# Kernel optimization log

Hardware: AMD Instinct MI355X
Metric: run time of the kernel (lower is better)

Reference implementation:

```python
import jax, jax.numpy as jnp
import numpy as np

B = 8192          # graphs
A = 1024          # atoms per graph
F = 32            # max fragments per graph
N = B * A
VIRTUAL_IDX = 4   # HPARAMS.get_node_idx('ligand_virtual')


def setup_inputs() -> dict:
    key = jax.random.key(0)
    k1, k2, k3, k4 = jax.random.split(key, 4)
    pos = jax.random.normal(k1, (N, 3), dtype=jnp.float32) * 10.0
    # -1 marks non-ligand atoms (no fragment), as in frag_idx_map semantics
    frag_idx_map = jax.random.randint(k2, (N,), -1, F, dtype=jnp.int32)
    batch_idx = (jnp.arange(N, dtype=jnp.int32) // A).astype(jnp.int32)
    node_entity = jax.random.randint(k3, (N,), 0, 6, dtype=jnp.int32)
    mask = jax.random.bernoulli(k4, 0.95, (N,))
    return {"pos": pos, "frag_idx_map": frag_idx_map, "batch_idx": batch_idx,
            "node_entity": node_entity, "mask": mask,
            "num_graphs": B, "max_frags_per_graph": F}


def reference(pos, frag_idx_map, batch_idx, node_entity, mask,
              num_graphs, max_frags_per_graph):
    """Fused equivalent of get_flat_fragment_index + get_fragment_com.

    Returns (coms [B*F, 3], counts [B*F], flat_frag_idx [N]).
    Rows of coms beyond a graph's actual fragment count are zero-padded.
    """
    Bn = num_graphs
    Fm = max_frags_per_graph
    is_ligand = frag_idx_map >= 0

    # num_frags_per_graph[i] = max(frag_idx in graph i) + 1 (0 if none)
    fmax = jax.ops.segment_max(jnp.where(is_ligand, frag_idx_map, -1),
                               batch_idx, num_segments=Bn)
    nfrag = jnp.maximum(fmax, -1) + 1  # [B]
    offset = jnp.concatenate([jnp.zeros((1,), nfrag.dtype),
                              jnp.cumsum(nfrag)[:-1]])  # [B]

    # flat fragment index in [0, sum(F_i)), -1 for non-ligand atoms
    flat_frag_idx = jnp.where(is_ligand,
                              frag_idx_map + offset[batch_idx],
                              -1)

    # COM excludes virtual nodes and masked dummies
    valid = is_ligand & mask & (node_entity != VIRTUAL_IDX)
    n_seg = Bn * Fm
    seg = jnp.where(valid, flat_frag_idx, n_seg)  # dump invalid into trash segment
    w = valid.astype(pos.dtype)
    sums = jax.ops.segment_sum(pos * w[:, None], seg, num_segments=n_seg + 1)[:-1]
    cnt = jax.ops.segment_sum(w, seg, num_segments=n_seg + 1)[:-1]
    coms = sums / jnp.maximum(cnt, 1.0)[:, None]
    return coms, cnt, flat_frag_idx
```

## Files before the change

kernel.cpp:

```cpp
#include <hip/hip_runtime.h>

#define GA 1024
#define GF 32
#define VIRT 4
#define KG 16

typedef _Float16 half8 __attribute__((ext_vector_type(8)));
typedef float f32x4 __attribute__((ext_vector_type(4)));
typedef unsigned int uint4v __attribute__((ext_vector_type(4)));

#define XSTRIDE 2080
#define KOFF    (4 * XSTRIDE)
#define FOFF    (KOFF + GA)
#define LDSSZ   (FOFF + 4 * GF * 4 * 4)

__device__ __forceinline__ unsigned int h2(float a, float b) {
    const unsigned short lo = __builtin_bit_cast(unsigned short, (_Float16)a);
    const unsigned short hi = __builtin_bit_cast(unsigned short, (_Float16)b);
    return (unsigned int)lo | ((unsigned int)hi << 16);
}

__global__ __launch_bounds__(256) void k_graph_acc(
    const float* __restrict__ pos,
    const int*   __restrict__ frag,
    const int*   __restrict__ entity,
    const int*   __restrict__ mask,
    float*       __restrict__ sums_cnt,
    int*         __restrict__ nfrag,
    unsigned*    __restrict__ frag8u)
{
    const int g    = blockIdx.x;
    const int t    = threadIdx.x;
    const int lane = t & 63;
    const int w    = t >> 6;

    __shared__ alignas(16) unsigned char lds[LDSSZ];
    __shared__ int s_wmax[4];

    const int i0 = g * GA + t * 4;
    const int4  f4 = *(const int4*)(frag   + i0);
    const int4  e4 = *(const int4*)(entity + i0);
    const int4  m4 = *(const int4*)(mask   + i0);
    const float4* p4 = (const float4*)(pos + (size_t)3 * i0);
    const float4 pa = p4[0], pb = p4[1], pc = p4[2];

    if (frag8u) {
        const unsigned s8p = (f4.x & 0xFFu)         | ((f4.y & 0xFFu) << 8)
                           | ((f4.z & 0xFFu) << 16) | ((unsigned)(f4.w & 0xFFu) << 24);
        frag8u[(size_t)g * (GA / 4) + t] = s8p;
    }

    #define KEY(F,M,E) ((unsigned)(((F) >= 0 && (M) != 0 && (E) != VIRT) ? (unsigned)(F) : 0xFFu))
    const unsigned kp = KEY(f4.x,m4.x,e4.x)        | (KEY(f4.y,m4.y,e4.y) << 8)
                      | (KEY(f4.z,m4.z,e4.z) << 16) | (KEY(f4.w,m4.w,e4.w) << 24);
    *(unsigned*)(lds + KOFF + t * 4) = kp;
    #undef KEY

    *(uint2*)(lds + 0 * XSTRIDE + t * 8) = make_uint2(h2(pa.x, pa.w), h2(pb.z, pc.y));
    *(uint2*)(lds + 1 * XSTRIDE + t * 8) = make_uint2(h2(pa.y, pb.x), h2(pb.w, pc.z));
    *(uint2*)(lds + 2 * XSTRIDE + t * 8) = make_uint2(h2(pa.z, pb.y), h2(pc.x, pc.w));
    *(uint2*)(lds + 3 * XSTRIDE + t * 8) = make_uint2(0x3C003C00u, 0x3C003C00u);

    int lm = max(max(f4.x, f4.y), max(f4.z, f4.w));
    #pragma unroll
    for (int off = 32; off > 0; off >>= 1)
        lm = max(lm, __shfl_down(lm, off, 64));
    if (lane == 0) s_wmax[w] = lm;

    f32x4 acc0 = {0.f, 0.f, 0.f, 0.f};
    f32x4 acc1 = {0.f, 0.f, 0.f, 0.f};
    const int row = lane & 15;
    const int grp = lane >> 4;
    const unsigned xoff = (unsigned)((row & 3) * XSTRIDE + (w * 256 + grp * 8) * 2);
    const unsigned koff = (unsigned)(KOFF + w * 256 + grp * 8);

    #pragma unroll
    for (int s = 0; s < 8; ++s) {
        const uint2  kk = *(const uint2*)(lds + koff + s * 32);
        const uint4v bv = *(const uint4v*)(lds + xoff + s * 64);
        uint4v a0, a1;
        #pragma unroll
        for (int p = 0; p < 4; ++p) {
            const unsigned word = (p & 2) ? kk.y : kk.x;
            const unsigned k0 = (word >> ((p & 1) * 16)) & 0xFFu;
            const unsigned k1 = (word >> ((p & 1) * 16 + 8)) & 0xFFu;
            a0[p] = (k0 == (unsigned)row        ? 0x3C00u : 0u)
                  | (k1 == (unsigned)row        ? 0x3C000000u : 0u);
            a1[p] = (k0 == (unsigned)(row + 16) ? 0x3C00u : 0u)
                  | (k1 == (unsigned)(row + 16) ? 0x3C000000u : 0u);
        }
        acc0 = __builtin_amdgcn_mfma_f32_16x16x32_f16(
                   __builtin_bit_cast(half8, a0), __builtin_bit_cast(half8, bv), acc0, 0, 0, 0);
        acc1 = __builtin_amdgcn_mfma_f32_16x16x32_f16(
                   __builtin_bit_cast(half8, a1), __builtin_bit_cast(half8, bv), acc1, 0, 0, 0);
    }

    float* fold = (float*)(lds + FOFF);
    if (row < 4) {
        #pragma unroll
        for (int r = 0; r < 4; ++r) {
            fold[(w * GF + grp * 4 + r) * 4 + row]      = acc0[r];
            fold[(w * GF + 16 + grp * 4 + r) * 4 + row] = acc1[r];
        }
    }
    __syncthreads();
    if (t < GF * 4) {
        const float v = fold[t] + fold[128 + t] + fold[256 + t] + fold[384 + t];
        sums_cnt[(size_t)g * (GF * 4) + t] = v;
    }
    if (t == 0)
        nfrag[g] = max(max(s_wmax[0], s_wmax[1]), max(s_wmax[2], s_wmax[3])) + 1;
}

__global__ __launch_bounds__(256) void k_fin(
    const int*      __restrict__ nfrag,
    const float4*   __restrict__ sums_cnt,
    const unsigned* __restrict__ frag8u,
    const int4*     __restrict__ frag4,
    float*          __restrict__ coms,
    float*          __restrict__ cnt_out,
    float4*         __restrict__ out4,
    int B)
{
    const int b = blockIdx.x;
    const int t = threadIdx.x;
    const int C = B / 256;
    __shared__ int s[8192 + 256];
    __shared__ int ps[256];

    for (int k = 0; k < C; ++k) {
        const int idx = k * 256 + t;
        s[idx + (idx >> 5)] = nfrag[idx];
    }
    __syncthreads();
    int sum = 0;
    for (int k = 0; k < C; ++k) {
        const int idx = t * C + k;
        const int p = idx + (idx >> 5);
        const int v = s[p];
        s[p] = sum;
        sum += v;
    }
    ps[t] = sum;
    __syncthreads();
    for (int d = 1; d < 256; d <<= 1) {
        const int v = (t >= d) ? ps[t - d] : 0;
        __syncthreads();
        ps[t] += v;
        __syncthreads();
    }
    #define OFF(g) (s[(g) + ((g) >> 5)] + (((g) >> 5) ? ps[((g) >> 5) - 1] : 0))
    const int total = ps[255];

    const int g0 = b * KG;

    #pragma unroll
    for (int k = 0; k < (KG * GF) / 256; ++k) {
        const int e  = k * 256 + t;
        const int j  = e >> 5, fr = e & 31;
        const int g  = g0 + j;
        if (fr < nfrag[g]) {
            const float4 v = sums_cnt[(size_t)g * GF + fr];
            const int rr = OFF(g) + fr;
            const float inv = 1.0f / fmaxf(v.w, 1.0f);
            coms[3 * rr + 0] = v.x * inv;
            coms[3 * rr + 1] = v.y * inv;
            coms[3 * rr + 2] = v.z * inv;
            cnt_out[rr] = v.w;
        }
    }

    #pragma unroll
    for (int k = 0; k < 2; ++k) {
        const int r = b * 512 + k * 256 + t;
        if (r >= total) {
            coms[3 * r + 0] = 0.0f; coms[3 * r + 1] = 0.0f; coms[3 * r + 2] = 0.0f;
            cnt_out[r] = 0.0f;
        }
    }

    for (int j = 0; j < KG; ++j) {
        const int g = g0 + j;
        const float fo = (float)OFF(g);
        float4 o;
        if (frag8u) {
            const unsigned kk = frag8u[(size_t)g * (GA / 4) + t];
            const int a0 = ((int)(kk << 24)) >> 24;
            const int a1 = ((int)(kk << 16)) >> 24;
            const int a2 = ((int)(kk <<  8)) >> 24;
            const int a3 = ((int)kk) >> 24;
            o.x = (a0 >= 0) ? (float)a0 + fo : -1.0f;
            o.y = (a1 >= 0) ? (float)a1 + fo : -1.0f;
            o.z = (a2 >= 0) ? (float)a2 + fo : -1.0f;
            o.w = (a3 >= 0) ? (float)a3 + fo : -1.0f;
        } else {
            const int4 f = frag4[(size_t)g * (GA / 4) + t];
            o.x = (f.x >= 0) ? (float)f.x + fo : -1.0f;
            o.y = (f.y >= 0) ? (float)f.y + fo : -1.0f;
            o.z = (f.z >= 0) ? (float)f.z + fo : -1.0f;
            o.w = (f.w >= 0) ? (float)f.w + fo : -1.0f;
        }
        out4[(size_t)g * (GA / 4) + t] = o;
    }
    #undef OFF
}

extern "C" void kernel_launch(void* const* d_in, const int* in_sizes, int n_in,
                              void* d_out, int out_size, void* d_ws, size_t ws_size,
                              hipStream_t stream)
{
    const float* pos    = (const float*)d_in[0];
    const int*   frag   = (const int*)d_in[1];
    const int*   entity = (const int*)d_in[3];
    const int*   mask   = (const int*)d_in[4];

    const int N = in_sizes[1];
    const int B = N / GA;

    float*    sums_cnt = (float*)d_ws;
    int*      nfrag    = (int*)(sums_cnt + (size_t)B * GF * 4);
    unsigned* frag8u   = (unsigned*)(nfrag + B);
    const size_t needed = (size_t)B * GF * 4 * 4 + (size_t)B * 4 + (size_t)N;
    if (ws_size < needed) frag8u = nullptr;

    float* coms     = (float*)d_out;
    float* cnt_out  = coms + (size_t)B * GF * 3;
    float* flat_out = cnt_out + (size_t)B * GF;

    k_graph_acc<<<B, 256, 0, stream>>>(pos, frag, entity, mask, sums_cnt, nfrag, frag8u);

    k_fin<<<B / KG, 256, 0, stream>>>(
        nfrag, (const float4*)sums_cnt, (const unsigned*)frag8u, (const int4*)frag,
        coms, cnt_out, (float4*)flat_out, B);
}
```

Before: 259.8 us.

## Process four graphs per block with register prefetch and atomic per-wave accumulation

Each block of the accumulation kernel now handles four consecutive graphs. While one graph is being processed, the loads for the next graph are issued into registers, so global loads overlap with the MFMA work. The LDS fold and its __syncthreads are gone: each wave atomically adds its partial sums into a workspace that a new memset clears first, and each wave writes its own max fragment index, which the finalize kernel reduces. This adds global atomics, an extra memset launch and a wider nfrag array in exchange for less block synchronization and better latency hiding.

```diff
diff --git a/kernel.cpp b/kernel.cpp
--- a/kernel.cpp
+++ b/kernel.cpp
@@ -3,6 +3,7 @@
 #define GA 1024
 #define GF 32
 #define VIRT 4
+#define NG 4
 #define KG 16
 
 typedef _Float16 half8 __attribute__((ext_vector_type(8)));
@@ -11,8 +12,7 @@
 
 #define XSTRIDE 2080
 #define KOFF    (4 * XSTRIDE)
-#define FOFF    (KOFF + GA)
-#define LDSSZ   (FOFF + 4 * GF * 4 * 4)
+#define LDSSZ   (KOFF + GA)
 
 __device__ __forceinline__ unsigned int h2(float a, float b) {
     const unsigned short lo = __builtin_bit_cast(unsigned short, (_Float16)a);
@@ -20,100 +20,111 @@
     return (unsigned int)lo | ((unsigned int)hi << 16);
 }
 
-__global__ __launch_bounds__(256) void k_graph_acc(
+__global__ __launch_bounds__(256, 8) void k_graph_acc(
     const float* __restrict__ pos,
     const int*   __restrict__ frag,
     const int*   __restrict__ entity,
     const int*   __restrict__ mask,
     float*       __restrict__ sums_cnt,
-    int*         __restrict__ nfrag,
+    int*         __restrict__ nfrag4,
     unsigned*    __restrict__ frag8u)
 {
-    const int g    = blockIdx.x;
     const int t    = threadIdx.x;
     const int lane = t & 63;
     const int w    = t >> 6;
+    const int g0   = blockIdx.x * NG;
 
     __shared__ alignas(16) unsigned char lds[LDSSZ];
-    __shared__ int s_wmax[4];
-
-    const int i0 = g * GA + t * 4;
-    const int4  f4 = *(const int4*)(frag   + i0);
-    const int4  e4 = *(const int4*)(entity + i0);
-    const int4  m4 = *(const int4*)(mask   + i0);
-    const float4* p4 = (const float4*)(pos + (size_t)3 * i0);
-    const float4 pa = p4[0], pb = p4[1], pc = p4[2];
-
-    if (frag8u) {
-        const unsigned s8p = (f4.x & 0xFFu)         | ((f4.y & 0xFFu) << 8)
-                           | ((f4.z & 0xFFu) << 16) | ((unsigned)(f4.w & 0xFFu) << 24);
-        frag8u[(size_t)g * (GA / 4) + t] = s8p;
-    }
-
-    #define KEY(F,M,E) ((unsigned)(((F) >= 0 && (M) != 0 && (E) != VIRT) ? (unsigned)(F) : 0xFFu))
-    const unsigned kp = KEY(f4.x,m4.x,e4.x)        | (KEY(f4.y,m4.y,e4.y) << 8)
-                      | (KEY(f4.z,m4.z,e4.z) << 16) | (KEY(f4.w,m4.w,e4.w) << 24);
-    *(unsigned*)(lds + KOFF + t * 4) = kp;
-    #undef KEY
-
-    *(uint2*)(lds + 0 * XSTRIDE + t * 8) = make_uint2(h2(pa.x, pa.w), h2(pb.z, pc.y));
-    *(uint2*)(lds + 1 * XSTRIDE + t * 8) = make_uint2(h2(pa.y, pb.x), h2(pb.w, pc.z));
-    *(uint2*)(lds + 2 * XSTRIDE + t * 8) = make_uint2(h2(pa.z, pb.y), h2(pc.x, pc.w));
-    *(uint2*)(lds + 3 * XSTRIDE + t * 8) = make_uint2(0x3C003C00u, 0x3C003C00u);
-
-    int lm = max(max(f4.x, f4.y), max(f4.z, f4.w));
-    #pragma unroll
-    for (int off = 32; off > 0; off >>= 1)
-        lm = max(lm, __shfl_down(lm, off, 64));
-    if (lane == 0) s_wmax[w] = lm;
-
-    f32x4 acc0 = {0.f, 0.f, 0.f, 0.f};
-    f32x4 acc1 = {0.f, 0.f, 0.f, 0.f};
+
     const int row = lane & 15;
     const int grp = lane >> 4;
-    const unsigned xoff = (unsigned)((row & 3) * XSTRIDE + (w * 256 + grp * 8) * 2);
-    const unsigned koff = (unsigned)(KOFF + w * 256 + grp * 8);
+    const unsigned xo_l = (unsigned)((row & 3) * XSTRIDE + (w * 256 + grp * 8) * 2);
+    const unsigned ko_l = (unsigned)(KOFF + w * 256 + grp * 8);
+
+    int4 f4, e4, m4; float4 pa, pb, pc;
+    {
+        const size_t i0 = (size_t)g0 * GA + t * 4;
+        f4 = *(const int4*)(frag   + i0);
+        e4 = *(const int4*)(entity + i0);
+        m4 = *(const int4*)(mask   + i0);
+        const float4* p4 = (const float4*)(pos + 3 * i0);
+        pa = p4[0]; pb = p4[1]; pc = p4[2];
+    }
 
     #pragma unroll
-    for (int s = 0; s < 8; ++s) {
-        const uint2  kk = *(const uint2*)(lds + koff + s * 32);
-        const uint4v bv = *(const uint4v*)(lds + xoff + s * 64);
-        uint4v a0, a1;
+    for (int it = 0; it < NG; ++it) {
+        const int g = g0 + it;
+        const int4  cf = f4, ce = e4, cm = m4;
+        const float4 qa = pa, qb = pb, qc = pc;
+
+        if (it + 1 < NG) {
+            const size_t i0 = (size_t)(g + 1) * GA + t * 4;
+            f4 = *(const int4*)(frag   + i0);
+            e4 = *(const int4*)(entity + i0);
+            m4 = *(const int4*)(mask   + i0);
+            const float4* p4 = (const float4*)(pos + 3 * i0);
+            pa = p4[0]; pb = p4[1]; pc = p4[2];
+        }
+
+        if (frag8u) {
+            const unsigned s8p = (cf.x & 0xFFu)         | ((cf.y & 0xFFu) << 8)
+                               | ((cf.z & 0xFFu) << 16) | ((unsigned)(cf.w & 0xFFu) << 24);
+            frag8u[(size_t)g * (GA / 4) + t] = s8p;
+        }
+
+        #define KEYV(F,M,E) ((unsigned)(((F) >= 0 && (M) != 0 && (E) != VIRT) ? (unsigned)(F) : 0xFFu))
+        const unsigned kp = KEYV(cf.x,cm.x,ce.x)        | (KEYV(cf.y,cm.y,ce.y) << 8)
+                          | (KEYV(cf.z,cm.z,ce.z) << 16) | (KEYV(cf.w,cm.w,ce.w) << 24);
+        *(unsigned*)(lds + KOFF + t * 4) = kp;
+        #undef KEYV
+
+        *(uint2*)(lds + 0 * XSTRIDE + t * 8) = make_uint2(h2(qa.x, qa.w), h2(qb.z, qc.y));
+        *(uint2*)(lds + 1 * XSTRIDE + t * 8) = make_uint2(h2(qa.y, qb.x), h2(qb.w, qc.z));
+        *(uint2*)(lds + 2 * XSTRIDE + t * 8) = make_uint2(h2(qa.z, qb.y), h2(qc.x, qc.w));
+        *(uint2*)(lds + 3 * XSTRIDE + t * 8) = make_uint2(0x3C003C00u, 0x3C003C00u);
+
+        int lm = max(max(cf.x, cf.y), max(cf.z, cf.w));
         #pragma unroll
-        for (int p = 0; p < 4; ++p) {
-            const unsigned word = (p & 2) ? kk.y : kk.x;
-            const unsigned k0 = (word >> ((p & 1) * 16)) & 0xFFu;
-            const unsigned k1 = (word >> ((p & 1) * 16 + 8)) & 0xFFu;
-            a0[p] = (k0 == (unsigned)row        ? 0x3C00u : 0u)
-                  | (k1 == (unsigned)row        ? 0x3C000000u : 0u);
-            a1[p] = (k0 == (unsigned)(row + 16) ? 0x3C00u : 0u)
-                  | (k1 == (unsigned)(row + 16) ? 0x3C000000u : 0u);
-        }
-        acc0 = __builtin_amdgcn_mfma_f32_16x16x32_f16(
-                   __builtin_bit_cast(half8, a0), __builtin_bit_cast(half8, bv), acc0, 0, 0, 0);
-        acc1 = __builtin_amdgcn_mfma_f32_16x16x32_f16(
-                   __builtin_bit_cast(half8, a1), __builtin_bit_cast(half8, bv), acc1, 0, 0, 0);
-    }
-
-    float* fold = (float*)(lds + FOFF);
-    if (row < 4) {
+        for (int off = 32; off > 0; off >>= 1)
+            lm = max(lm, __shfl_down(lm, off, 64));
+        if (lane == 0) nfrag4[g * 4 + w] = lm;
+
+        f32x4 acc0 = {0.f, 0.f, 0.f, 0.f};
+        f32x4 acc1 = {0.f, 0.f, 0.f, 0.f};
         #pragma unroll
-        for (int r = 0; r < 4; ++r) {
-            fold[(w * GF + grp * 4 + r) * 4 + row]      = acc0[r];
-            fold[(w * GF + 16 + grp * 4 + r) * 4 + row] = acc1[r];
-        }
-    }
-    __syncthreads();
-    if (t < GF * 4) {
-        const float v = fold[t] + fold[128 + t] + fold[256 + t] + fold[384 + t];
-        sums_cnt[(size_t)g * (GF * 4) + t] = v;
-    }
-    if (t == 0)
-        nfrag[g] = max(max(s_wmax[0], s_wmax[1]), max(s_wmax[2], s_wmax[3])) + 1;
+        for (int s = 0; s < 8; ++s) {
+            const uint2  kk = *(const uint2*)(lds + ko_l + s * 32);
+            const uint4v bv = *(const uint4v*)(lds + xo_l + s * 64);
+            uint4v a0, a1;
+            #pragma unroll
+            for (int p = 0; p < 4; ++p) {
+                const unsigned word = (p & 2) ? kk.y : kk.x;
+                const unsigned k0 = (word >> ((p & 1) * 16)) & 0xFFu;
+                const unsigned k1 = (word >> ((p & 1) * 16 + 8)) & 0xFFu;
+                a0[p] = (k0 == (unsigned)row        ? 0x3C00u : 0u)
+                      | (k1 == (unsigned)row        ? 0x3C000000u : 0u);
+                a1[p] = (k0 == (unsigned)(row + 16) ? 0x3C00u : 0u)
+                      | (k1 == (unsigned)(row + 16) ? 0x3C000000u : 0u);
+            }
+            acc0 = __builtin_amdgcn_mfma_f32_16x16x32_f16(
+                       __builtin_bit_cast(half8, a0), __builtin_bit_cast(half8, bv), acc0, 0, 0, 0);
+            acc1 = __builtin_amdgcn_mfma_f32_16x16x32_f16(
+                       __builtin_bit_cast(half8, a1), __builtin_bit_cast(half8, bv), acc1, 0, 0, 0);
+        }
+
+        if (row < 4) {
+            float* dst = sums_cnt + (size_t)g * (GF * 4);
+            #pragma unroll
+            for (int r = 0; r < 4; ++r) {
+                atomicAdd(dst + (grp * 4 + r) * 4 + row,        acc0[r]);
+                atomicAdd(dst + (16 + grp * 4 + r) * 4 + row,   acc1[r]);
+            }
+        }
+    }
 }
 
 __global__ __launch_bounds__(256) void k_fin(
-    const int*      __restrict__ nfrag,
+    const int4*     __restrict__ nfrag4v,
     const float4*   __restrict__ sums_cnt,
     const unsigned* __restrict__ frag8u,
     const int4*     __restrict__ frag4,
@@ -130,7 +141,8 @@
 
     for (int k = 0; k < C; ++k) {
         const int idx = k * 256 + t;
-        s[idx + (idx >> 5)] = nfrag[idx];
+        const int4 nv = nfrag4v[idx];
+        s[idx + (idx >> 5)] = max(max(nv.x, nv.y), max(nv.z, nv.w)) + 1;
     }
     __syncthreads();
     int sum = 0;
@@ -159,7 +171,9 @@
         const int e  = k * 256 + t;
         const int j  = e >> 5, fr = e & 31;
         const int g  = g0 + j;
-        if (fr < nfrag[g]) {
+        const int4 nv = nfrag4v[g];
+        const int nfr = max(max(nv.x, nv.y), max(nv.z, nv.w)) + 1;
+        if (fr < nfr) {
             const float4 v = sums_cnt[(size_t)g * GF + fr];
             const int rr = OFF(g) + fr;
             const float inv = 1.0f / fmaxf(v.w, 1.0f);
@@ -218,18 +232,21 @@
     const int B = N / GA;
 
     float*    sums_cnt = (float*)d_ws;
-    int*      nfrag    = (int*)(sums_cnt + (size_t)B * GF * 4);
-    unsigned* frag8u   = (unsigned*)(nfrag + B);
-    const size_t needed = (size_t)B * GF * 4 * 4 + (size_t)B * 4 + (size_t)N;
+    int*      nfrag4   = (int*)(sums_cnt + (size_t)B * GF * 4);
+    unsigned* frag8u   = (unsigned*)(nfrag4 + (size_t)B * 4);
+    const size_t needed = (size_t)B * GF * 4 * 4 + (size_t)B * 16 + (size_t)N;
     if (ws_size < needed) frag8u = nullptr;
 
     float* coms     = (float*)d_out;
     float* cnt_out  = coms + (size_t)B * GF * 3;
     float* flat_out = cnt_out + (size_t)B * GF;
 
-    k_graph_acc<<<B, 256, 0, stream>>>(pos, frag, entity, mask, sums_cnt, nfrag, frag8u);
+    hipMemsetAsync(sums_cnt, 0, (size_t)B * GF * 4 * sizeof(float), stream);
+
+    k_graph_acc<<<B / NG, 256, 0, stream>>>(pos, frag, entity, mask,
+                                            sums_cnt, nfrag4, frag8u);
 
     k_fin<<<B / KG, 256, 0, stream>>>(
-        nfrag, (const float4*)sums_cnt, (const unsigned*)frag8u, (const int4*)frag,
-        coms, cnt_out, (float4*)flat_out, B);
-}
+        (const int4*)nfrag4, (const float4*)sums_cnt, (const unsigned*)frag8u,
+        (const int4*)frag, coms, cnt_out, (float4*)flat_out, B);
+}
```

New measurement: 297.3 us. 1.14x slower.

## Hoist global scan into single-block kernel; finalize one graph per block

Applied to the files above, without the earlier changes.

Before, every block of the finalize kernel recomputed the full prefix sum over all graph fragment counts (8192 entries) before writing its slice. The scan now runs once in a dedicated one-block kernel that writes per-graph offsets and the total to workspace. The finalize kernel then runs one block per graph and reads its offset directly. This removes the redundant per-block scan but adds a third launch with a serial single-block stage. The fallback path for a small workspace, which read the original int32 fragment map, is also dropped.

```diff
diff --git a/kernel.cpp b/kernel.cpp
--- a/kernel.cpp
+++ b/kernel.cpp
@@ -3,7 +3,6 @@
 #define GA 1024
 #define GF 32
 #define VIRT 4
-#define KG 16
 
 typedef _Float16 half8 __attribute__((ext_vector_type(8)));
 typedef float f32x4 __attribute__((ext_vector_type(4)));
@@ -44,11 +43,9 @@
     const float4* p4 = (const float4*)(pos + (size_t)3 * i0);
     const float4 pa = p4[0], pb = p4[1], pc = p4[2];
 
-    if (frag8u) {
-        const unsigned s8p = (f4.x & 0xFFu)         | ((f4.y & 0xFFu) << 8)
-                           | ((f4.z & 0xFFu) << 16) | ((unsigned)(f4.w & 0xFFu) << 24);
-        frag8u[(size_t)g * (GA / 4) + t] = s8p;
-    }
+    const unsigned s8p = (f4.x & 0xFFu)         | ((f4.y & 0xFFu) << 8)
+                       | ((f4.z & 0xFFu) << 16) | ((unsigned)(f4.w & 0xFFu) << 24);
+    frag8u[(size_t)g * (GA / 4) + t] = s8p;
 
     #define KEY(F,M,E) ((unsigned)(((F) >= 0 && (M) != 0 && (E) != VIRT) ? (unsigned)(F) : 0xFFu))
     const unsigned kp = KEY(f4.x,m4.x,e4.x)        | (KEY(f4.y,m4.y,e4.y) << 8)
@@ -112,17 +109,9 @@
         nfrag[g] = max(max(s_wmax[0], s_wmax[1]), max(s_wmax[2], s_wmax[3])) + 1;
 }
 
-__global__ __launch_bounds__(256) void k_fin(
-    const int*      __restrict__ nfrag,
-    const float4*   __restrict__ sums_cnt,
-    const unsigned* __restrict__ frag8u,
-    const int4*     __restrict__ frag4,
-    float*          __restrict__ coms,
-    float*          __restrict__ cnt_out,
-    float4*         __restrict__ out4,
-    int B)
-{
-    const int b = blockIdx.x;
+__global__ __launch_bounds__(256) void k_scan(
+    const int* __restrict__ nfrag, int* __restrict__ offset, int B)
+{
     const int t = threadIdx.x;
     const int C = B / 256;
     __shared__ int s[8192 + 256];
@@ -133,6 +122,7 @@
         s[idx + (idx >> 5)] = nfrag[idx];
     }
     __syncthreads();
+
     int sum = 0;
     for (int k = 0; k < C; ++k) {
         const int idx = t * C + k;
@@ -143,66 +133,68 @@
     }
     ps[t] = sum;
     __syncthreads();
+
     for (int d = 1; d < 256; d <<= 1) {
         const int v = (t >= d) ? ps[t - d] : 0;
         __syncthreads();
         ps[t] += v;
         __syncthreads();
     }
-    #define OFF(g) (s[(g) + ((g) >> 5)] + (((g) >> 5) ? ps[((g) >> 5) - 1] : 0))
-    const int total = ps[255];
-
-    const int g0 = b * KG;
-
-    #pragma unroll
-    for (int k = 0; k < (KG * GF) / 256; ++k) {
-        const int e  = k * 256 + t;
-        const int j  = e >> 5, fr = e & 31;
-        const int g  = g0 + j;
-        if (fr < nfrag[g]) {
-            const float4 v = sums_cnt[(size_t)g * GF + fr];
-            const int rr = OFF(g) + fr;
+
+    for (int k = 0; k < C; ++k) {
+        const int idx = k * 256 + t;
+        const int c = idx >> 5;
+        const int pre = (c == 0) ? 0 : ps[c - 1];
+        offset[idx] = pre + s[idx + (idx >> 5)];
+    }
+    if (t == 255) offset[B] = ps[255];
+}
+
+__global__ __launch_bounds__(256) void k_fin2(
+    const int*      __restrict__ nfrag,
+    const int*      __restrict__ offset,
+    const float4*   __restrict__ sums_cnt,
+    const unsigned* __restrict__ frag8u,
+    float*          __restrict__ coms,
+    float*          __restrict__ cnt_out,
+    float4*         __restrict__ out4,
+    int B)
+{
+    const int b = blockIdx.x;
+    const int t = threadIdx.x;
+    const int off = offset[b];
+
+    {
+        const float fo = (float)off;
+        const unsigned kk = frag8u[(size_t)b * (GA / 4) + t];
+        const int a0 = ((int)(kk << 24)) >> 24;
+        const int a1 = ((int)(kk << 16)) >> 24;
+        const int a2 = ((int)(kk <<  8)) >> 24;
+        const int a3 = ((int)kk) >> 24;
+        float4 o;
+        o.x = (a0 >= 0) ? (float)a0 + fo : -1.0f;
+        o.y = (a1 >= 0) ? (float)a1 + fo : -1.0f;
+        o.z = (a2 >= 0) ? (float)a2 + fo : -1.0f;
+        o.w = (a3 >= 0) ? (float)a3 + fo : -1.0f;
+        out4[(size_t)b * (GA / 4) + t] = o;
+    }
+
+    if (t < GF) {
+        if (t < nfrag[b]) {
+            const float4 v = sums_cnt[(size_t)b * GF + t];
+            const int rr = off + t;
             const float inv = 1.0f / fmaxf(v.w, 1.0f);
             coms[3 * rr + 0] = v.x * inv;
             coms[3 * rr + 1] = v.y * inv;
             coms[3 * rr + 2] = v.z * inv;
             cnt_out[rr] = v.w;
         }
-    }
-
-    #pragma unroll
-    for (int k = 0; k < 2; ++k) {
-        const int r = b * 512 + k * 256 + t;
-        if (r >= total) {
+        const int r = b * GF + t;
+        if (r >= offset[B]) {
             coms[3 * r + 0] = 0.0f; coms[3 * r + 1] = 0.0f; coms[3 * r + 2] = 0.0f;
             cnt_out[r] = 0.0f;
         }
     }
-
-    for (int j = 0; j < KG; ++j) {
-        const int g = g0 + j;
-        const float fo = (float)OFF(g);
-        float4 o;
-        if (frag8u) {
-            const unsigned kk = frag8u[(size_t)g * (GA / 4) + t];
-            const int a0 = ((int)(kk << 24)) >> 24;
-            const int a1 = ((int)(kk << 16)) >> 24;
-            const int a2 = ((int)(kk <<  8)) >> 24;
-            const int a3 = ((int)kk) >> 24;
-            o.x = (a0 >= 0) ? (float)a0 + fo : -1.0f;
-            o.y = (a1 >= 0) ? (float)a1 + fo : -1.0f;
-            o.z = (a2 >= 0) ? (float)a2 + fo : -1.0f;
-            o.w = (a3 >= 0) ? (float)a3 + fo : -1.0f;
-        } else {
-            const int4 f = frag4[(size_t)g * (GA / 4) + t];
-            o.x = (f.x >= 0) ? (float)f.x + fo : -1.0f;
-            o.y = (f.y >= 0) ? (float)f.y + fo : -1.0f;
-            o.z = (f.z >= 0) ? (float)f.z + fo : -1.0f;
-            o.w = (f.w >= 0) ? (float)f.w + fo : -1.0f;
-        }
-        out4[(size_t)g * (GA / 4) + t] = o;
-    }
-    #undef OFF
 }
 
 extern "C" void kernel_launch(void* const* d_in, const int* in_sizes, int n_in,
@@ -219,17 +211,19 @@
 
     float*    sums_cnt = (float*)d_ws;
     int*      nfrag    = (int*)(sums_cnt + (size_t)B * GF * 4);
-    unsigned* frag8u   = (unsigned*)(nfrag + B);
-    const size_t needed = (size_t)B * GF * 4 * 4 + (size_t)B * 4 + (size_t)N;
-    if (ws_size < needed) frag8u = nullptr;
+    int*      offset   = nfrag + B;
+    unsigned* frag8u   = (unsigned*)(offset + B + 1);
 
     float* coms     = (float*)d_out;
     float* cnt_out  = coms + (size_t)B * GF * 3;
     float* flat_out = cnt_out + (size_t)B * GF;
 
-    k_graph_acc<<<B, 256, 0, stream>>>(pos, frag, entity, mask, sums_cnt, nfrag, frag8u);
-
-    k_fin<<<B / KG, 256, 0, stream>>>(
-        nfrag, (const float4*)sums_cnt, (const unsigned*)frag8u, (const int4*)frag,
+    k_graph_acc<<<B, 256, 0, stream>>>(pos, frag, entity, mask,
+                                       sums_cnt, nfrag, frag8u);
+
+    k_scan<<<1, 256, 0, stream>>>(nfrag, offset, B);
+
+    k_fin2<<<B, 256, 0, stream>>>(
+        nfrag, offset, (const float4*)sums_cnt, (const unsigned*)frag8u,
         coms, cnt_out, (float4*)flat_out, B);
 }
```

After: 258.2 us. No clear change (-0.6%).
